# Kernel tuning notes

Hardware: AMD Instinct MI355X
Metric: run time of the kernel (lower is better)

## Reference

```python
import jax, jax.numpy as jnp
import numpy as np

DIM = 1024
MULT = 4
HID = DIM * MULT
E = 8
B, S = 2, 2048


def _rmsnorm(x):
    # zeta SimpleRMSNorm: F.normalize(x, dim=-1) * sqrt(dim)
    n = jnp.linalg.norm(x, axis=-1, keepdims=True)
    return x / jnp.maximum(n, 1e-12) * jnp.sqrt(jnp.asarray(x.shape[-1], x.dtype))


def _act_quant(x):
    # per-token 8-bit absmax quant (BitNet b1.58), straight-through in fwd math
    scale = 127.0 / jnp.clip(jnp.max(jnp.abs(x), axis=-1, keepdims=True), 1e-5)
    q = jnp.clip(jnp.round(x * scale), -128, 127) / scale
    return x + jax.lax.stop_gradient(q - x)


def _w_quant(w, axes):
    # ternary weight quant with per-matrix mean-abs scale
    scale = 1.0 / jnp.clip(jnp.mean(jnp.abs(w), axis=axes, keepdims=True), 1e-5)
    q = jnp.clip(jnp.round(w * scale), -1, 1) / scale
    return w + jax.lax.stop_gradient(q - w)


def setup_inputs() -> dict:
    key = jax.random.key(0)
    ks = jax.random.split(key, 8)
    sd = 0.02
    x = jax.random.normal(ks[0], (B, S, DIM), dtype=jnp.float32)
    gw = jax.random.normal(ks[1], (E, DIM), dtype=jnp.float32) * sd
    gb = jnp.zeros((E,), dtype=jnp.float32)
    w1 = jax.random.normal(ks[2], (E, HID, DIM), dtype=jnp.float32) * sd
    b1 = jnp.zeros((E, HID), dtype=jnp.float32)
    w2 = jax.random.normal(ks[3], (E, DIM, HID), dtype=jnp.float32) * sd
    b2 = jnp.zeros((E, DIM), dtype=jnp.float32)
    return {"x": x, "gw": gw, "gb": gb, "w1": w1, "b1": b1, "w2": w2, "b2": b2}


def reference(x, gw, gb, w1, b1, w2, b2):
    # BitLinear input preprocessing: RMSNorm then 8-bit activation quant
    xq = _act_quant(_rmsnorm(x))  # [B,S,D]

    # Gate: softmax(BitLinear(dim, E))
    logits = jnp.einsum("bsd,ed->bse", xq, _w_quant(gw, axes=(0, 1))) + gb
    gates = jax.nn.softmax(logits, axis=-1)  # [B,S,E]

    # Experts: BitLinear -> GELU -> BitLinear, quant scales per expert
    w1q = _w_quant(w1, axes=(1, 2))  # [E,H,D]
    w2q = _w_quant(w2, axes=(1, 2))  # [E,D,H]
    h = jnp.einsum("bsd,ehd->bseh", xq, w1q) + b1  # [B,S,E,H]
    a = jax.nn.gelu(h, approximate=False)
    aq = _act_quant(_rmsnorm(a))
    expert_out = jnp.einsum("bseh,edh->bsed", aq, w2q) + b2  # [B,S,E,D]

    # softmax-weighted sum over experts
    return jnp.einsum("bse,bsed->bsd", gates, expert_out)
```

## Files before the change

### kernel.cpp

```cpp
#include <hip/hip_runtime.h>


#define T_TOK 4096
#define DIMS  1024
#define HID   4096
#define NE    8
#define ROWB  8192ull

typedef __attribute__((ext_vector_type(4))) int       i32x4;
typedef __attribute__((ext_vector_type(8))) _Float16  f16x8;

__device__ __forceinline__ float block_sum(float v, float* buf, int tid) {
  #pragma unroll
  for (int o = 32; o > 0; o >>= 1) v += __shfl_down(v, o, 64);
  __syncthreads();
  if ((tid & 63) == 0) buf[tid >> 6] = v;
  __syncthreads();
  return buf[0] + buf[1] + buf[2] + buf[3];
}
__device__ __forceinline__ float block_max(float v, float* buf, int tid) {
  #pragma unroll
  for (int o = 32; o > 0; o >>= 1) { float t = __shfl_down(v, o, 64); v = fmaxf(v, t); }
  __syncthreads();
  if ((tid & 63) == 0) buf[tid >> 6] = v;
  __syncthreads();
  return fmaxf(fmaxf(buf[0], buf[1]), fmaxf(buf[2], buf[3]));
}

__device__ __forceinline__ void gl_lds16(const void* g, void* l) {
  __builtin_amdgcn_global_load_lds(
      (const __attribute__((address_space(1))) unsigned int*)g,
      (__attribute__((address_space(3))) unsigned int*)l, 16, 0, 0);
}

__device__ __forceinline__ int q8(float v) {
  return ((int)fminf(fmaxf(rintf(v), -128.0f), 127.0f)) & 0xff;
}

__device__ __forceinline__ float erf_fast(float x) {
  const float ax = fabsf(x);
  const float t = __builtin_amdgcn_rcpf(fmaf(0.3275911f, ax, 1.0f));
  float p = fmaf(1.061405429f, t, -1.453152027f);
  p = fmaf(p, t, 1.421413741f);
  p = fmaf(p, t, -0.284496736f);
  p = fmaf(p, t, 0.254829592f);
  p = p * t;
  const float e = __expf(-ax * ax);
  const float r = fmaf(-p, e, 1.0f);
  return copysignf(r, x);
}
__device__ __forceinline__ float gelu_fast(float h) {
  return 0.5f * h * (1.0f + erf_fast(h * 0.70710678118654752f));
}

__global__ __launch_bounds__(256) void wabs_sum_kernel(
    const float4* __restrict__ w, int n_f4, int shift, float* __restrict__ sums) {
  __shared__ float buf[4];
  const int tid = threadIdx.x;
  const int base = blockIdx.x * 4096;
  float acc = 0.0f;
  for (int k = 0; k < 16; ++k) {
    int fi = base + k * 256 + tid;
    if (fi < n_f4) {
      float4 v = w[fi];
      acc += fabsf(v.x) + fabsf(v.y) + fabsf(v.z) + fabsf(v.w);
    }
  }
  acc = block_sum(acc, buf, tid);
  if (tid == 0) atomicAdd(&sums[base >> shift], acc);
}

__global__ void mkscales_kernel(const float* __restrict__ wsum, float* __restrict__ sc) {
  if (threadIdx.x == 0) {
    #pragma unroll
    for (int e = 0; e < NE; ++e) {
      float m1 = fmaxf(wsum[e] * (1.0f / 4194304.0f), 1e-5f);
      sc[e] = m1; sc[8 + e] = 1.0f / m1;
      float m2 = fmaxf(wsum[8 + e] * (1.0f / 4194304.0f), 1e-5f);
      sc[16 + e] = m2; sc[24 + e] = 1.0f / m2;
    }
    float mg = fmaxf(wsum[16] * (1.0f / 8192.0f), 1e-5f);
    sc[32] = mg; sc[33] = 1.0f / mg;
  }
}

__global__ __launch_bounds__(256) void wquant_kernel(
    const float4* __restrict__ w, int* __restrict__ o, int n_f4, int shift,
    const float* __restrict__ qs) {
  int fi = blockIdx.x * 256 + threadIdx.x;
  if (fi >= n_f4) return;
  const float s = qs[fi >> shift];
  float4 v = w[fi];
  int b0 = ((int)fminf(fmaxf(rintf(v.x * s), -1.0f), 1.0f)) & 0xff;
  int b1 = ((int)fminf(fmaxf(rintf(v.y * s), -1.0f), 1.0f)) & 0xff;
  int b2 = ((int)fminf(fmaxf(rintf(v.z * s), -1.0f), 1.0f)) & 0xff;
  int b3 = ((int)fminf(fmaxf(rintf(v.w * s), -1.0f), 1.0f)) & 0xff;
  o[fi] = b0 | (b1 << 8) | (b2 << 16) | (b3 << 24);
}

__global__ __launch_bounds__(256) void preprocess_kernel(
    const float* __restrict__ x, const float* __restrict__ gw,
    const float* __restrict__ gb, const float* __restrict__ scales,
    int* __restrict__ qx, float* __restrict__ inv_sx, float* __restrict__ gates) {
  __shared__ float buf[4];
  const int t = blockIdx.x, tid = threadIdx.x;
  const float4 xv = ((const float4*)(x + (size_t)t * DIMS))[tid];
  float ss = xv.x * xv.x + xv.y * xv.y + xv.z * xv.z + xv.w * xv.w;
  ss = block_sum(ss, buf, tid);
  const float rr = 32.0f / fmaxf(sqrtf(ss), 1e-12f);
  const float y0 = xv.x * rr, y1 = xv.y * rr, y2 = xv.z * rr, y3 = xv.w * rr;
  float am = fmaxf(fmaxf(fabsf(y0), fabsf(y1)), fmaxf(fabsf(y2), fabsf(y3)));
  am = block_max(am, buf, tid);
  const float aclip = fmaxf(am, 1e-5f);
  const float qsc = 127.0f / aclip;
  const float q0 = fminf(fmaxf(rintf(y0 * qsc), -128.0f), 127.0f);
  const float q1 = fminf(fmaxf(rintf(y1 * qsc), -128.0f), 127.0f);
  const float q2 = fminf(fmaxf(rintf(y2 * qsc), -128.0f), 127.0f);
  const float q3 = fminf(fmaxf(rintf(y3 * qsc), -128.0f), 127.0f);
  qx[t * 256 + tid] = (((int)q0) & 0xff) | ((((int)q1) & 0xff) << 8) |
                      ((((int)q2) & 0xff) << 16) | ((((int)q3) & 0xff) << 24);

  const float gqs = scales[33];
  float lg[NE];
  #pragma unroll
  for (int e = 0; e < NE; ++e) {
    const float4 gv = ((const float4*)(gw + e * DIMS))[tid];
    float t0 = fminf(fmaxf(rintf(gv.x * gqs), -1.0f), 1.0f);
    float t1 = fminf(fmaxf(rintf(gv.y * gqs), -1.0f), 1.0f);
    float t2 = fminf(fmaxf(rintf(gv.z * gqs), -1.0f), 1.0f);
    float t3 = fminf(fmaxf(rintf(gv.w * gqs), -1.0f), 1.0f);
    lg[e] = q0 * t0 + q1 * t1 + q2 * t2 + q3 * t3;
  }
  #pragma unroll
  for (int e = 0; e < NE; ++e) lg[e] = block_sum(lg[e], buf, tid);
  if (tid == 0) {
    const float gsabs = scales[32];
    const float isx = aclip / 127.0f;
    inv_sx[t] = isx;
    float l[NE], mx = -1e30f;
    #pragma unroll
    for (int e = 0; e < NE; ++e) { l[e] = lg[e] * (isx * gsabs) + gb[e]; mx = fmaxf(mx, l[e]); }
    float s = 0.0f;
    #pragma unroll
    for (int e = 0; e < NE; ++e) { l[e] = expf(l[e] - mx); s += l[e]; }
    const float inv = 1.0f / s;
    #pragma unroll
    for (int e = 0; e < NE; ++e) gates[t * NE + e] = l[e] * inv;
  }
}

template <int SA, int SB, int NT>
__device__ __forceinline__ void gemm_core_i8(
    const char* __restrict__ A, const char* __restrict__ Bm,
    int m0, int n0, char* sA, char* sB, i32x4 (&acc)[8][4]) {
  const int tid = threadIdx.x;
  const int lane = tid & 63;
  const int lm = lane & 15, lq = lane >> 4;
  const int wv = tid >> 6;
  const int wr = (wv >> 2) * 128, wc = (wv & 3) * 64;

  const int c0 = tid, c1 = 512 + tid;
  const int r0 = c0 >> 2, r1 = c1 >> 2;
  const int g0 = ((c0 & 3) ^ ((r0 >> 1) & 3)) << 4;
  const int g1 = ((c1 & 3) ^ ((r1 >> 1) & 3)) << 4;
  const char* gA0 = A + (size_t)(m0 + r0) * SA + g0;
  const char* gA1 = A + (size_t)(m0 + r1) * SA + g1;
  const char* gB0 = Bm + (size_t)(n0 + r0) * SB + g0;
  const char* gB1 = Bm + (size_t)(n0 + r1) * SB + g1;
  const int l0 = c0 * 16, l1 = c1 * 16;

  const int swz = (lq ^ ((lm >> 1) & 3)) << 4;
  const int aoff = (wr + lm) * 64 + swz;
  const int boff = (wc + lm) * 64 + swz;

#define STAGE_I8(j)                                           \
  do {                                                        \
    const int _b = (j) & 3; const int _k = (j) * 64;          \
    gl_lds16(gA0 + _k, sA + _b * 16384 + l0);                 \
    gl_lds16(gA1 + _k, sA + _b * 16384 + l1);                 \
    gl_lds16(gB0 + _k, sB + _b * 16384 + l0);                 \
    gl_lds16(gB1 + _k, sB + _b * 16384 + l1);                 \
  } while (0)

  STAGE_I8(0); STAGE_I8(1); STAGE_I8(2);
  asm volatile("s_waitcnt vmcnt(8)" ::: "memory");
  __builtin_amdgcn_s_barrier();
  asm volatile("" ::: "memory");

  for (int t = 0; t < NT; ++t) {
    const int cur = t & 3;
    if (t + 3 < NT) STAGE_I8(t + 3);
    const char* bA = sA + cur * 16384;
    const char* bB = sB + cur * 16384;
    i32x4 av[8], bv[4];
    #pragma unroll
    for (int i = 0; i < 8; ++i) av[i] = *(const i32x4*)(bA + aoff + i * 1024);
    #pragma unroll
    for (int j = 0; j < 4; ++j) bv[j] = *(const i32x4*)(bB + boff + j * 1024);
    __builtin_amdgcn_s_setprio(1);
    #pragma unroll
    for (int i = 0; i < 8; ++i)
      #pragma unroll
      for (int j = 0; j < 4; ++j)
        acc[i][j] = __builtin_amdgcn_mfma_i32_16x16x64_i8(av[i], bv[j], acc[i][j], 0, 0, 0);
    __builtin_amdgcn_s_setprio(0);
    if (t < NT - 1) {
      if (t + 3 < NT)       { asm volatile("s_waitcnt vmcnt(8)" ::: "memory"); }
      else if (t + 3 == NT) { asm volatile("s_waitcnt vmcnt(4)" ::: "memory"); }
      else                  { asm volatile("s_waitcnt vmcnt(0)" ::: "memory"); }
      __builtin_amdgcn_s_barrier();
      asm volatile("" ::: "memory");
    }
  }
#undef STAGE_I8
}

__global__ __launch_bounds__(512, 2) void gemm1_kernel(
    const char* __restrict__ qx, const char* __restrict__ w1q,
    const float* __restrict__ scales, const float* __restrict__ inv_sx,
    const float* __restrict__ b1, char* __restrict__ aqa) {
  __shared__ __align__(16) char sA[4 * 16384];
  __shared__ __align__(16) char sB[4 * 16384];
  const int wg = blockIdx.x;
  const int e = wg & 7;
  const int i2 = wg >> 3;
  const int yi = i2 & 15, xi = i2 >> 4;
  const int m0 = yi * 256, n0 = xi * 256;
  const char* Bm = w1q + (size_t)e * HID * DIMS;
  i32x4 acc[8][4] = {};
  gemm_core_i8<DIMS, DIMS, DIMS / 64>(qx, Bm, m0, n0, sA, sB, acc);

  const int tid = threadIdx.x, lane = tid & 63, wv = tid >> 6;
  const int wr = (wv >> 2) * 128, wc = (wv & 3) * 64, lm = lane & 15, lq = lane >> 4;
  char* obase = aqa + (size_t)e * T_TOK * ROWB;
  const float s1 = scales[e];
  float bb[4];
  #pragma unroll
  for (int j = 0; j < 4; ++j) bb[j] = b1[e * HID + n0 + wc + j * 16 + lm];
  #pragma unroll
  for (int i = 0; i < 8; ++i) {
    #pragma unroll
    for (int r = 0; r < 4; ++r) {
      const int row = m0 + wr + i * 16 + lq * 4 + r;
      const float rs = inv_sx[row] * s1;
      _Float16* orow = (_Float16*)(obase + (size_t)row * ROWB);
      #pragma unroll
      for (int j = 0; j < 4; ++j) {
        const int col = n0 + wc + j * 16 + lm;
        orow[col] = (_Float16)fmaf((float)acc[i][j][r], rs, bb[j]);
      }
    }
  }
}

__global__ __launch_bounds__(256) void rowquant_kernel(
    char* __restrict__ aqa, float* __restrict__ inv_sa) {
  __shared__ float buf[4];
  const size_t R = blockIdx.x;
  char* rowb = aqa + R * ROWB;
  const int tid = threadIdx.x;
  f16x8 v0 = ((const f16x8*)rowb)[tid * 2];
  f16x8 v1 = ((const f16x8*)rowb)[tid * 2 + 1];
  float f[16];
  #pragma unroll
  for (int k = 0; k < 8; ++k) { f[k] = (float)v0[k]; f[8 + k] = (float)v1[k]; }
  #pragma unroll
  for (int k = 0; k < 16; ++k) f[k] = gelu_fast(f[k]);
  float ss = 0.0f;
  #pragma unroll
  for (int k = 0; k < 16; ++k) ss += f[k] * f[k];
  ss = block_sum(ss, buf, tid);
  const float rr = 64.0f / fmaxf(sqrtf(ss), 1e-12f);
  float am = 0.0f;
  #pragma unroll
  for (int k = 0; k < 16; ++k) am = fmaxf(am, fabsf(f[k] * rr));
  am = block_max(am, buf, tid);
  const float aclip = fmaxf(am, 1e-5f);
  const float qsc = rr * 127.0f / aclip;
  int4 o;
  o.x = q8(f[0] * qsc) | (q8(f[1] * qsc) << 8) | (q8(f[2] * qsc) << 16) | (q8(f[3] * qsc) << 24);
  o.y = q8(f[4] * qsc) | (q8(f[5] * qsc) << 8) | (q8(f[6] * qsc) << 16) | (q8(f[7] * qsc) << 24);
  o.z = q8(f[8] * qsc) | (q8(f[9] * qsc) << 8) | (q8(f[10] * qsc) << 16) | (q8(f[11] * qsc) << 24);
  o.w = q8(f[12] * qsc) | (q8(f[13] * qsc) << 8) | (q8(f[14] * qsc) << 16) | (q8(f[15] * qsc) << 24);
  ((int4*)rowb)[tid] = o;
  if (tid == 0) inv_sa[R] = aclip / 127.0f;
}

__global__ __launch_bounds__(512, 2) void gemm2_kernel(
    const char* __restrict__ aqa, const char* __restrict__ w2q,
    const float* __restrict__ scales, const float* __restrict__ inv_sa,
    const float* __restrict__ b2, const float* __restrict__ gates,
    void* __restrict__ dstv, int use_atomic) {
  __shared__ __align__(16) char sA[4 * 16384];
  __shared__ __align__(16) char sB[4 * 16384];
  const int wg = blockIdx.x;
  const int e = wg & 7;
  const int i2 = wg >> 3;
  const int xi = i2 & 3, yi = i2 >> 2;
  const int m0 = yi * 256, n0 = xi * 256;
  const char* A = aqa + (size_t)e * T_TOK * ROWB;
  const char* Bm = w2q + (size_t)e * DIMS * HID;
  i32x4 acc[8][4] = {};
  gemm_core_i8<(int)ROWB, HID, HID / 64>(A, Bm, m0, n0, sA, sB, acc);

  const int tid = threadIdx.x, lane = tid & 63, wv = tid >> 6;
  const int wr = (wv >> 2) * 128, wc = (wv & 3) * 64, lm = lane & 15, lq = lane >> 4;
  const float s2 = scales[16 + e];
  float bb[4];
  #pragma unroll
  for (int j = 0; j < 4; ++j) bb[j] = b2[e * DIMS + n0 + wc + j * 16 + lm];
  #pragma unroll
  for (int i = 0; i < 8; ++i) {
    #pragma unroll
    for (int r = 0; r < 4; ++r) {
      const int row = m0 + wr + i * 16 + lq * 4 + r;
      const float rs = inv_sa[(size_t)e * T_TOK + row] * s2;
      const float g = gates[row * NE + e];
      #pragma unroll
      for (int j = 0; j < 4; ++j) {
        const int col = n0 + wc + j * 16 + lm;
        const float v = g * fmaf((float)acc[i][j][r], rs, bb[j]);
        if (use_atomic) atomicAdd(&((float*)dstv)[(size_t)row * DIMS + col], v);
        else ((_Float16*)dstv)[((size_t)e * T_TOK + row) * DIMS + col] = (_Float16)v;
      }
    }
  }
}

__global__ __launch_bounds__(256) void reduce_kernel(
    const f16x8* __restrict__ eout, float4* __restrict__ out) {
  const int i = blockIdx.x * 256 + threadIdx.x;
  float s[8] = {};
  #pragma unroll
  for (int e = 0; e < NE; ++e) {
    f16x8 v = eout[(size_t)e * (T_TOK * DIMS / 8) + i];
    #pragma unroll
    for (int k = 0; k < 8; ++k) s[k] += (float)v[k];
  }
  float4 o0; o0.x = s[0]; o0.y = s[1]; o0.z = s[2]; o0.w = s[3];
  float4 o1; o1.x = s[4]; o1.y = s[5]; o1.z = s[6]; o1.w = s[7];
  out[i * 2]     = o0;
  out[i * 2 + 1] = o1;
}

extern "C" void kernel_launch(void* const* d_in, const int* in_sizes, int n_in,
                              void* d_out, int out_size, void* d_ws, size_t ws_size,
                              hipStream_t stream) {
  const float* x  = (const float*)d_in[0];
  const float* gw = (const float*)d_in[1];
  const float* gb = (const float*)d_in[2];
  const float* w1 = (const float*)d_in[3];
  const float* b1 = (const float*)d_in[4];
  const float* w2 = (const float*)d_in[5];
  const float* b2 = (const float*)d_in[6];
  float* outp = (float*)d_out;
  char* ws = (char*)d_ws;

  float* wsum   = (float*)(ws + 0);
  float* scales = (float*)(ws + 256);
  float* inv_sx = (float*)(ws + 4096);
  float* gates  = (float*)(ws + 20480);
  float* inv_sa = (float*)(ws + 151552);
  char*  qx     = ws + 282624;
  char*  w1q    = ws + 4476928;
  char*  w2q    = ws + 38031360;
  char*  aqa    = ws + 71585792;
  char*  eout   = ws + 340021248;

  const bool has_eout = ws_size >= 340021248ull + 67108864ull;

  hipMemsetAsync(wsum, 0, 17 * sizeof(float), stream);
  wabs_sum_kernel<<<2048, 256, 0, stream>>>((const float4*)w1, 8388608, 20, wsum + 0);
  wabs_sum_kernel<<<2048, 256, 0, stream>>>((const float4*)w2, 8388608, 20, wsum + 8);
  wabs_sum_kernel<<<1,    256, 0, stream>>>((const float4*)gw, 2048,    30, wsum + 16);
  mkscales_kernel<<<1, 64, 0, stream>>>(wsum, scales);
  wquant_kernel<<<32768, 256, 0, stream>>>((const float4*)w1, (int*)w1q, 8388608, 20, scales + 8);
  wquant_kernel<<<32768, 256, 0, stream>>>((const float4*)w2, (int*)w2q, 8388608, 20, scales + 24);
  preprocess_kernel<<<4096, 256, 0, stream>>>(x, gw, gb, scales, (int*)qx, inv_sx, gates);

  gemm1_kernel<<<2048, 512, 0, stream>>>(qx, w1q, scales, inv_sx, b1, aqa);
  rowquant_kernel<<<32768, 256, 0, stream>>>(aqa, inv_sa);

  if (has_eout) {
    gemm2_kernel<<<512, 512, 0, stream>>>(
        aqa, w2q, scales, inv_sa, b2, gates, eout, 0);
    reduce_kernel<<<2048, 256, 0, stream>>>((const f16x8*)eout, (float4*)outp);
  } else {
    hipMemsetAsync(outp, 0, (size_t)out_size * sizeof(float), stream);
    gemm2_kernel<<<512, 512, 0, stream>>>(
        aqa, w2q, scales, inv_sa, b2, gates, outp, 1);
  }
}
```

Measured before the change: 938.2 us.

## Split int8 GEMM K-step into two phases interleaving LDS reads, prefetch and MFMA

Restructures the int8 MFMA main loop so each K-tile is processed in two halves. The first half of the A fragments is read from LDS, then half of the next global-to-LDS prefetch is issued and the first MFMA group runs, followed by the same for the second half. The aim is to overlap LDS reads and global loads with MFMA work and cut register pressure from holding all eight A fragments. It adds extra workgroup barriers per iteration, which could add synchronisation stalls.

```diff
diff --git a/kernel.cpp b/kernel.cpp
--- a/kernel.cpp
+++ b/kernel.cpp
@@ -173,46 +173,66 @@
   const int aoff = (wr + lm) * 64 + swz;
   const int boff = (wc + lm) * 64 + swz;
 
-#define STAGE_I8(j)                                           \
+#define STAGE_LO(j)                                           \
   do {                                                        \
     const int _b = (j) & 3; const int _k = (j) * 64;          \
     gl_lds16(gA0 + _k, sA + _b * 16384 + l0);                 \
+    gl_lds16(gB0 + _k, sB + _b * 16384 + l0);                 \
+  } while (0)
+#define STAGE_HI(j)                                           \
+  do {                                                        \
+    const int _b = (j) & 3; const int _k = (j) * 64;          \
     gl_lds16(gA1 + _k, sA + _b * 16384 + l1);                 \
-    gl_lds16(gB0 + _k, sB + _b * 16384 + l0);                 \
     gl_lds16(gB1 + _k, sB + _b * 16384 + l1);                 \
   } while (0)
 
-  STAGE_I8(0); STAGE_I8(1); STAGE_I8(2);
+  STAGE_LO(0); STAGE_HI(0);
+  STAGE_LO(1); STAGE_HI(1);
+  STAGE_LO(2); STAGE_HI(2);
   asm volatile("s_waitcnt vmcnt(8)" ::: "memory");
   __builtin_amdgcn_s_barrier();
   asm volatile("" ::: "memory");
 
   for (int t = 0; t < NT; ++t) {
-    const int cur = t & 3;
-    if (t + 3 < NT) STAGE_I8(t + 3);
-    const char* bA = sA + cur * 16384;
-    const char* bB = sB + cur * 16384;
-    i32x4 av[8], bv[4];
-    #pragma unroll
-    for (int i = 0; i < 8; ++i) av[i] = *(const i32x4*)(bA + aoff + i * 1024);
+    const char* bA = sA + (t & 3) * 16384;
+    const char* bB = sB + (t & 3) * 16384;
+    i32x4 avl[4], avh[4], bv[4];
+    #pragma unroll
+    for (int i = 0; i < 4; ++i) avl[i] = *(const i32x4*)(bA + aoff + i * 1024);
     #pragma unroll
     for (int j = 0; j < 4; ++j) bv[j] = *(const i32x4*)(bB + boff + j * 1024);
+    if (t + 3 < NT) STAGE_LO(t + 3);
+    __builtin_amdgcn_s_barrier();
+    asm volatile("s_waitcnt lgkmcnt(0)" ::: "memory");
     __builtin_amdgcn_s_setprio(1);
     #pragma unroll
-    for (int i = 0; i < 8; ++i)
+    for (int i = 0; i < 4; ++i)
       #pragma unroll
       for (int j = 0; j < 4; ++j)
-        acc[i][j] = __builtin_amdgcn_mfma_i32_16x16x64_i8(av[i], bv[j], acc[i][j], 0, 0, 0);
+        acc[i][j] = __builtin_amdgcn_mfma_i32_16x16x64_i8(avl[i], bv[j], acc[i][j], 0, 0, 0);
     __builtin_amdgcn_s_setprio(0);
-    if (t < NT - 1) {
-      if (t + 3 < NT)       { asm volatile("s_waitcnt vmcnt(8)" ::: "memory"); }
-      else if (t + 3 == NT) { asm volatile("s_waitcnt vmcnt(4)" ::: "memory"); }
-      else                  { asm volatile("s_waitcnt vmcnt(0)" ::: "memory"); }
-      __builtin_amdgcn_s_barrier();
-      asm volatile("" ::: "memory");
-    }
-  }
-#undef STAGE_I8
+    __builtin_amdgcn_s_barrier();
+    asm volatile("" ::: "memory");
+    #pragma unroll
+    for (int i = 0; i < 4; ++i) avh[i] = *(const i32x4*)(bA + aoff + (4 + i) * 1024);
+    if (t + 3 < NT) STAGE_HI(t + 3);
+    if (t + 3 < NT)      { asm volatile("s_waitcnt vmcnt(8)" ::: "memory"); }
+    else if (t + 2 < NT) { asm volatile("s_waitcnt vmcnt(4)" ::: "memory"); }
+    else                 { asm volatile("s_waitcnt vmcnt(0)" ::: "memory"); }
+    __builtin_amdgcn_s_barrier();
+    asm volatile("s_waitcnt lgkmcnt(0)" ::: "memory");
+    __builtin_amdgcn_s_setprio(1);
+    #pragma unroll
+    for (int i = 0; i < 4; ++i)
+      #pragma unroll
+      for (int j = 0; j < 4; ++j)
+        acc[4 + i][j] = __builtin_amdgcn_mfma_i32_16x16x64_i8(avh[i], bv[j], acc[4 + i][j], 0, 0, 0);
+    __builtin_amdgcn_s_setprio(0);
+    __builtin_amdgcn_s_barrier();
+    asm volatile("" ::: "memory");
+  }
+#undef STAGE_LO
+#undef STAGE_HI
 }
 
 __global__ __launch_bounds__(512, 2) void gemm1_kernel(
```

Result: no change. 927.5 us (-1.1%).
